# Kernel optimization log

Hardware: AMD Instinct MI355X
Metric: run time of the kernel (lower is better)

## Reference

```python
import jax, jax.numpy as jnp
import numpy as np

B, N, H = 32, 1024, 128
EPS = 1e-5


def setup_inputs() -> dict:
    key = jax.random.key(0)
    ks = jax.random.split(key, 9)
    node_embeddings = jax.random.normal(ks[0], (B, N, H), dtype=jnp.float32)
    edge_relations = jax.random.normal(ks[1], (B, N, N, 3), dtype=jnp.float32)
    adjacency = jax.random.randint(ks[2], (N, N), 0, 2, dtype=jnp.int32)
    s_msg = 1.0 / np.sqrt(H + 3)
    s_upd = 1.0 / np.sqrt(2 * H)
    W_msg = jax.random.uniform(ks[3], (H, H + 3), jnp.float32, -s_msg, s_msg)
    b_msg = jax.random.uniform(ks[4], (H,), jnp.float32, -s_msg, s_msg)
    W_upd = jax.random.uniform(ks[5], (H, 2 * H), jnp.float32, -s_upd, s_upd)
    b_upd = jax.random.uniform(ks[6], (H,), jnp.float32, -s_upd, s_upd)
    gamma = jnp.ones((H,), jnp.float32)
    beta = jnp.zeros((H,), jnp.float32)
    return {"node_embeddings": node_embeddings, "edge_relations": edge_relations,
            "adjacency": adjacency, "W_msg": W_msg, "b_msg": b_msg,
            "W_upd": W_upd, "b_upd": b_upd, "gamma": gamma, "beta": beta}


def reference(node_embeddings, edge_relations, adjacency, W_msg, b_msg, W_upd, b_upd, gamma, beta):
    # node_embeddings: [B,N,H]; edge_relations: [B,N,N,3]; adjacency: [N,N]
    b_, n_, h_ = node_embeddings.shape
    mask = (adjacency > 0).astype(node_embeddings.dtype)  # mask[j,i]=1 if i is neighbor of j
    # Split msg_nn weight: Linear(cat(h_i, e_ij)) = h_i @ W_h^T + e_ij @ W_e^T + b
    W_h = W_msg[:, :h_]   # [H,H]
    W_e = W_msg[:, h_:]   # [H,3]
    h_part = jnp.einsum('bih,oh->bio', node_embeddings, W_h)       # [B,N,H]
    msg_h = jnp.einsum('ji,bio->bjo', mask, h_part)                # aggregate sender linear part
    e_agg = jnp.einsum('bijc,ji->bjc', edge_relations, mask)       # aggregate edge feats first (memory-bound)
    msg_e = jnp.einsum('bjc,oc->bjo', e_agg, W_e)
    deg = mask.sum(axis=1)                                         # [N] in-degree of j
    messages = msg_h + msg_e + deg[None, :, None] * b_msg          # bias added once per edge
    # Dropout(0.2) is identity in inference; BatchNorm uses batch stats (training-mode math).
    upd_in = jnp.concatenate([node_embeddings, messages], axis=-1)  # [B,N,2H]
    updated = jax.nn.relu(jnp.einsum('bjk,ok->bjo', upd_in, W_upd) + b_upd)
    flat = updated.reshape(-1, h_)
    mean = flat.mean(axis=0)
    var = flat.var(axis=0)  # biased, as BatchNorm1d
    normed = (flat - mean) * jax.lax.rsqrt(var + EPS) * gamma + beta
    return normed.reshape(b_, n_, h_) + node_embeddings
```

## Files before the change

kernel.cpp:

```cpp
#include <hip/hip_runtime.h>

typedef _Float16 f16;
typedef f16 f16x4 __attribute__((ext_vector_type(4)));
typedef f16 f16x8 __attribute__((ext_vector_type(8)));
typedef float f32x4 __attribute__((ext_vector_type(4)));

#define BB 32
#define NN 1024
#define HH 128
#define ROWS (BB*NN)
#define EPS 1e-5f

__device__ __forceinline__ f16 f2h(float x) { return (f16)x; }

typedef __attribute__((address_space(1))) const void gv_t;
typedef __attribute__((address_space(3))) void lv_t;
__device__ __forceinline__ void gl_lds16(const void* g, void* l) {
  __builtin_amdgcn_global_load_lds((gv_t*)g, (lv_t*)l, 16, 0, 0);
}

__global__ __launch_bounds__(256) void prep0_k(
    const float* __restrict__ W_msg, const float* __restrict__ W_upd,
    const float* __restrict__ node, const int* __restrict__ adj,
    f16* __restrict__ Wh, f16* __restrict__ Wupd, float* __restrict__ We,
    f16* __restrict__ nodeh, f16* __restrict__ maskf, f16* __restrict__ maskT,
    float* __restrict__ e_agg, float* __restrict__ sums)
{
  const int blk = blockIdx.x, t = threadIdx.x;
  if (blk < 64) {
    const long base = (long)blk*16384 + t;
    #pragma unroll
    for (int p = 0; p < 64; p++) {
      const long idx = base + (long)p*256;
      const float4 v = ((const float4*)node)[idx];
      f16x4 hv; hv[0] = f2h(v.x); hv[1] = f2h(v.y); hv[2] = f2h(v.z); hv[3] = f2h(v.w);
      *(f16x4*)&nodeh[idx << 2] = hv;
    }
  } else if (blk < 128) {
    __shared__ f16 ldsT[128][136];
    const int tt = blk - 64, tj = tt >> 3, ti = tt & 7;
    #pragma unroll
    for (int p = 0; p < 16; p++) {
      const int q = p*256 + t;
      const int row = q >> 5, c4 = (q & 31) << 2;
      const int4 m = *(const int4*)&adj[(long)(tj*128 + row)*NN + ti*128 + c4];
      f16x4 hv;
      hv[0] = (m.x > 0) ? (f16)1.0f : (f16)0.0f;
      hv[1] = (m.y > 0) ? (f16)1.0f : (f16)0.0f;
      hv[2] = (m.z > 0) ? (f16)1.0f : (f16)0.0f;
      hv[3] = (m.w > 0) ? (f16)1.0f : (f16)0.0f;
      *(f16x4*)&maskf[(long)(tj*128 + row)*NN + ti*128 + c4] = hv;
      ldsT[c4 + 0][row] = hv[0];
      ldsT[c4 + 1][row] = hv[1];
      ldsT[c4 + 2][row] = hv[2];
      ldsT[c4 + 3][row] = hv[3];
    }
    __syncthreads();
    #pragma unroll
    for (int p = 0; p < 8; p++) {
      const int q = p*256 + t;
      const int rT = q >> 4, c8 = (q & 15) << 3;
      *(uint4*)&maskT[(long)(ti*128 + rT)*NN + tj*128 + c8] =
          *(const uint4*)&ldsT[rT][c8];
    }
  } else if (blk == 128) {
    for (int idx = t; idx < HH*HH; idx += 256) {
      const int o = idx >> 7, h = idx & 127;
      Wh[idx] = f2h(W_msg[o*131 + h]);
    }
  } else if (blk == 129) {
    for (int idx = t; idx < HH*256; idx += 256)
      Wupd[idx] = f2h(W_upd[idx]);
  } else if (blk == 130) {
    for (int idx = t; idx < HH*3; idx += 256)
      We[idx] = W_msg[(idx/3)*131 + 128 + (idx % 3)];
    if (t < 256) sums[t] = 0.f;
  } else {
    const int base = (blk - 131) * 24576 + t;
    #pragma unroll
    for (int r = 0; r < 96; r++) e_agg[base + r*256] = 0.f;
  }
}

__global__ __launch_bounds__(256) void phaseB_k(
    const f16* __restrict__ nodeh, const float* __restrict__ E,
    const f16* __restrict__ maskT, const f16* __restrict__ Wh,
    const float* __restrict__ b_msg,
    f16* __restrict__ h_part_T, float* __restrict__ e_agg)
{
  __shared__ __align__(16) char smem[16384];
  const int tid = threadIdx.x;

  if (blockIdx.x >= 256) {
    const int e   = blockIdx.x - 256;
    const int bb  = e / 96;
    const int rem = e - bb*96;
    const int seg = rem >> 5;
    const int ic  = rem & 31;
    const int i0  = ic << 5;
    const int p0  = (seg << 10) + (tid << 2);
    const int j0  = p0 / 3;
    const int r   = p0 - j0*3;
    const bool s1 = (r >= 2);
    const bool s2 = (r >= 1);
    const float* Ep = E + (long)bb*3145728 + (long)i0*3072 + p0;
    const f16*   Mp = maskT + (long)i0*NN + j0;
    float a0 = 0.f, a1 = 0.f, a2 = 0.f, a3 = 0.f;
    for (int c8 = 0; c8 < 4; c8++) {
      float4 ev[8];
      float m0v[8], m1v[8];
      #pragma unroll
      for (int v = 0; v < 8; v++)
        ev[v] = *(const float4*)(Ep + (long)(c8*8 + v)*3072);
      #pragma unroll
      for (int v = 0; v < 8; v++) {
        const long moff = (long)(c8*8 + v)*NN;
        m0v[v] = (float)Mp[moff];
        m1v[v] = (float)Mp[moff + 1];
      }
      #pragma unroll
      for (int v = 0; v < 8; v++) {
        a0 = fmaf(m0v[v],              ev[v].x, a0);
        a1 = fmaf(s1 ? m1v[v] : m0v[v], ev[v].y, a1);
        a2 = fmaf(s2 ? m1v[v] : m0v[v], ev[v].z, a2);
        a3 = fmaf(m1v[v],              ev[v].w, a3);
      }
    }
    float* ebp = e_agg + (long)bb*3072 + p0;
    atomicAdd(ebp,     a0);
    atomicAdd(ebp + 1, a1);
    atomicAdd(ebp + 2, a2);
    atomicAdd(ebp + 3, a3);
    return;
  }

  f16* As = (f16*)smem;
  f16* Bs = (f16*)(smem + 8192);
  const int g  = blockIdx.x;
  const int nt = g & 7, bb = g >> 3;
  const int nbase = nt << 7;
  const int lane = tid & 63, wave = tid >> 6;
  const int wm = (wave & 1) << 6, wn = (wave >> 1) << 6;

  f32x4 acc[2][4], acc2[2][4];
  #pragma unroll
  for (int i = 0; i < 2; i++)
    #pragma unroll
    for (int j = 0; j < 4; j++)
      #pragma unroll
      for (int r = 0; r < 4; r++) { acc[i][j][r] = 0.f; acc2[i][j][r] = 0.f; }

  for (int k0 = 0; k0 < HH; k0 += 32) {
    #pragma unroll
    for (int p = 0; p < 2; p++) {
      const int q = (p << 8) + tid;
      const int row = q >> 2, kp = (q & 3) << 3;
      gl_lds16(&Wh[(long)row*HH + k0 + kp], &As[q << 3]);
      gl_lds16(&nodeh[(long)((bb << 10) + nbase + row)*HH + k0 + kp], &Bs[q << 3]);
    }
    __syncthreads();
    f16x8 af[4], bf[4];
    #pragma unroll
    for (int i = 0; i < 4; i++) {
      af[i] = *(const f16x8*)&As[((wm + (i << 4) + (lane & 15)) << 5) + ((lane >> 4) << 3)];
      bf[i] = *(const f16x8*)&Bs[((wn + (i << 4) + (lane & 15)) << 5) + ((lane >> 4) << 3)];
    }
    #pragma unroll
    for (int i = 0; i < 2; i++)
      #pragma unroll
      for (int j = 0; j < 4; j++) {
        acc[i][j]  = __builtin_amdgcn_mfma_f32_16x16x32_f16(af[i],     bf[j], acc[i][j],  0, 0, 0);
        acc2[i][j] = __builtin_amdgcn_mfma_f32_16x16x32_f16(af[i + 2], bf[j], acc2[i][j], 0, 0, 0);
      }
    __syncthreads();
  }

  f16* out = h_part_T + (long)bb * (HH*NN);
  const int rb = (lane >> 4) << 2, cb = lane & 15;
  #pragma unroll
  for (int i = 0; i < 4; i++)
    #pragma unroll
    for (int r = 0; r < 4; r++) {
      const int gm = wm + (i << 4) + rb + r;
      const float bm = b_msg[gm];
      #pragma unroll
      for (int j = 0; j < 4; j++) {
        const int gn = nbase + wn + (j << 4) + cb;
        const float v = ((i < 2) ? acc[i][j][r] : acc2[i - 2][j][r]) + bm;
        out[(long)gm*NN + gn] = f2h(v);
      }
    }
}

__global__ __launch_bounds__(256) void gemm12_k(
    const f16* __restrict__ maskf, const f16* __restrict__ hp,
    const float* __restrict__ e_agg, const float* __restrict__ We,
    const f16* __restrict__ nodeh, const f16* __restrict__ Wupd,
    const float* __restrict__ b_upd,
    f16* __restrict__ upd, float* __restrict__ sums)
{
  const int mt = blockIdx.x, bb = blockIdx.z;
  const int jb = mt << 7;
  const long rowb = (long)bb*NN + jb;
  __shared__ f16 As[128*32];
  __shared__ f16 Bs[128*32];
  __shared__ __align__(16) char msgs_lds[128*128*2];
  __shared__ float colS[128], colQ[128];
  const int tid = threadIdx.x, lane = tid & 63, wave = tid >> 6;
  const int wm = (wave & 1) << 6, wn = (wave >> 1) << 6;
  if (tid < 128) { colS[tid] = 0.f; colQ[tid] = 0.f; }
  const int rb = (lane >> 4) << 2, cb = lane & 15;

  f32x4 acc[4][4];
  #pragma unroll
  for (int i = 0; i < 4; i++)
    #pragma unroll
    for (int j = 0; j < 4; j++)
      #pragma unroll
      for (int r = 0; r < 4; r++) acc[i][j][r] = 0.f;

  for (int k0 = 0; k0 < NN; k0 += 32) {
    #pragma unroll
    for (int p = 0; p < 2; p++) {
      const int q = (p << 8) + tid;
      const int row = q >> 2, kp = (q & 3) << 3;
      gl_lds16(&maskf[(long)(jb + row)*NN + k0 + kp], &As[q << 3]);
      gl_lds16(&hp[(long)bb*(HH*NN) + (long)row*NN + k0 + kp], &Bs[q << 3]);
    }
    __syncthreads();
    f16x8 af[4], bf[4];
    #pragma unroll
    for (int i = 0; i < 4; i++) {
      af[i] = *(const f16x8*)&As[((wm + (i << 4) + (lane & 15)) << 5) + ((lane >> 4) << 3)];
      bf[i] = *(const f16x8*)&Bs[((wn + (i << 4) + (lane & 15)) << 5) + ((lane >> 4) << 3)];
    }
    #pragma unroll
    for (int i = 0; i < 4; i++)
      #pragma unroll
      for (int j = 0; j < 4; j++)
        acc[i][j] = __builtin_amdgcn_mfma_f32_16x16x32_f16(af[i], bf[j], acc[i][j], 0, 0, 0);
    __syncthreads();
  }

  #pragma unroll
  for (int i = 0; i < 4; i++)
    #pragma unroll
    for (int r = 0; r < 4; r++) {
      const int lrow = wm + (i << 4) + rb + r;
      const long eb = (rowb + lrow)*3;
      const float e0 = e_agg[eb], e1 = e_agg[eb+1], e2 = e_agg[eb+2];
      #pragma unroll
      for (int j = 0; j < 4; j++) {
        const int col = wn + (j << 4) + cb;
        const float v = acc[i][j][r]
                      + e0*We[col*3] + e1*We[col*3+1] + e2*We[col*3+2];
        const int byte = ((lrow << 8) + (col << 1)) ^ ((lrow & 7) << 4);
        *(f16*)(msgs_lds + byte) = f2h(v);
      }
    }
  __syncthreads();

  f32x4 acc2[4][4];
  #pragma unroll
  for (int i = 0; i < 4; i++)
    #pragma unroll
    for (int j = 0; j < 4; j++)
      #pragma unroll
      for (int r = 0; r < 4; r++) acc2[i][j][r] = 0.f;

  for (int k0 = 0; k0 < 256; k0 += 32) {
    const bool fromA = (k0 < HH);
    #pragma unroll
    for (int p = 0; p < 2; p++) {
      const int q = (p << 8) + tid;
      const int row = q >> 2, kp = (q & 3) << 3;
      if (fromA)
        gl_lds16(&nodeh[(rowb + row)*HH + k0 + kp], &As[q << 3]);
      gl_lds16(&Wupd[(long)row*256 + k0 + kp], &Bs[q << 3]);
    }
    __syncthreads();
    f16x8 af[4], bf[4];
    #pragma unroll
    for (int i = 0; i < 4; i++) {
      if (fromA) {
        af[i] = *(const f16x8*)&As[((wm + (i << 4) + (lane & 15)) << 5) + ((lane >> 4) << 3)];
      } else {
        const int lrow = wm + (i << 4) + (lane & 15);
        const int byte = ((lrow << 8) + (((k0 - HH) + ((lane >> 4) << 3)) << 1))
                         ^ ((lrow & 7) << 4);
        af[i] = *(const f16x8*)(msgs_lds + byte);
      }
      bf[i] = *(const f16x8*)&Bs[((wn + (i << 4) + (lane & 15)) << 5) + ((lane >> 4) << 3)];
    }
    #pragma unroll
    for (int i = 0; i < 4; i++)
      #pragma unroll
      for (int j = 0; j < 4; j++)
        acc2[i][j] = __builtin_amdgcn_mfma_f32_16x16x32_f16(af[i], bf[j], acc2[i][j], 0, 0, 0);
    __syncthreads();
  }

  float bup[4], s[4] = {0,0,0,0}, qq[4] = {0,0,0,0};
  #pragma unroll
  for (int j = 0; j < 4; j++) bup[j] = b_upd[wn + (j << 4) + cb];
  #pragma unroll
  for (int i = 0; i < 4; i++)
    #pragma unroll
    for (int r = 0; r < 4; r++) {
      const long gm = rowb + wm + (i << 4) + rb + r;
      #pragma unroll
      for (int j = 0; j < 4; j++) {
        const int gn = wn + (j << 4) + cb;
        const float v = fmaxf(acc2[i][j][r] + bup[j], 0.f);
        upd[gm*HH + gn] = f2h(v);
        s[j] += v; qq[j] += v*v;
      }
    }
  #pragma unroll
  for (int j = 0; j < 4; j++) {
    const int gn = wn + (j << 4) + cb;
    atomicAdd(&colS[gn], s[j]);
    atomicAdd(&colQ[gn], qq[j]);
  }
  __syncthreads();
  if (tid < 128) {
    atomicAdd(&sums[tid],       colS[tid]);
    atomicAdd(&sums[128 + tid], colQ[tid]);
  }
}

__global__ __launch_bounds__(256) void final_k(const f16* __restrict__ upd,
    const float* __restrict__ node, const float* __restrict__ sums,
    const float* __restrict__ gamma, const float* __restrict__ beta,
    float* __restrict__ out)
{
  const long idx = (long)blockIdx.x*256 + threadIdx.x;
  const f16x4 u  = *(const f16x4*)&upd[idx << 2];
  const float4 nd = ((const float4*)node)[idx];
  const int ob = (idx & 31) << 2;
  const float inv = 1.0f/32768.0f;
  float4 res;
  #pragma unroll
  for (int c = 0; c < 4; c++) {
    const float m  = sums[ob + c]*inv;
    const float va = sums[128 + ob + c]*inv - m*m;
    const float sc = rsqrtf(va + EPS)*gamma[ob + c];
    ((float*)&res)[c] = ((float)u[c] - m)*sc + beta[ob + c]
                      + ((const float*)&nd)[c];
  }
  ((float4*)out)[idx] = res;
}

extern "C" void kernel_launch(void* const* d_in, const int* in_sizes, int n_in,
                              void* d_out, int out_size, void* d_ws, size_t ws_size,
                              hipStream_t stream) {
  const float* node  = (const float*)d_in[0];
  const float* E     = (const float*)d_in[1];
  const int*   adj   = (const int*)  d_in[2];
  const float* W_msg = (const float*)d_in[3];
  const float* b_msg = (const float*)d_in[4];
  const float* W_upd = (const float*)d_in[5];
  const float* b_upd = (const float*)d_in[6];
  const float* gamma = (const float*)d_in[7];
  const float* beta  = (const float*)d_in[8];
  float* out = (float*)d_out;

  char* p = (char*)d_ws;
  auto alloc = [&](size_t n) { void* r = (void*)p; p += (n + 255) & ~(size_t)255; return r; };
  f16*   h_part_T = (f16*)  alloc((size_t)BB*HH*NN*2);
  f16*   upd      = (f16*)  alloc((size_t)ROWS*HH*2);
  f16*   nodeh    = (f16*)  alloc((size_t)ROWS*HH*2);
  f16*   maskf    = (f16*)  alloc((size_t)NN*NN*2);
  f16*   maskT    = (f16*)  alloc((size_t)NN*NN*2);
  float* e_agg    = (float*)alloc((size_t)BB*NN*3*4);
  f16*   Wh       = (f16*)  alloc((size_t)HH*HH*2);
  f16*   Wupd     = (f16*)  alloc((size_t)HH*256*2);
  float* We       = (float*)alloc((size_t)HH*3*4);
  float* sums     = (float*)alloc((size_t)256*4);

  prep0_k<<<135, 256, 0, stream>>>(W_msg, W_upd, node, adj,
                                   Wh, Wupd, We, nodeh, maskf, maskT,
                                   e_agg, sums);

  phaseB_k<<<3328, 256, 0, stream>>>(nodeh, E, maskT, Wh, b_msg, h_part_T, e_agg);

  gemm12_k<<<dim3(8, 1, BB), 256, 0, stream>>>(maskf, h_part_T, e_agg, We,
                                               nodeh, Wupd, b_upd, upd, sums);

  final_k<<<4096, 256, 0, stream>>>(upd, node, sums, gamma, beta, out);
}
```

Baseline: 624.8 us.

## Double-buffer LDS tiles in gemm12 and halve edge-aggregation block count

```diff
diff --git a/kernel.cpp b/kernel.cpp
--- a/kernel.cpp
+++ b/kernel.cpp
@@ -93,11 +93,11 @@
 
   if (blockIdx.x >= 256) {
     const int e   = blockIdx.x - 256;
-    const int bb  = e / 96;
-    const int rem = e - bb*96;
-    const int seg = rem >> 5;
-    const int ic  = rem & 31;
-    const int i0  = ic << 5;
+    const int bb  = e / 48;
+    const int rem = e - bb*48;
+    const int seg = rem >> 4;
+    const int ic  = rem & 15;
+    const int i0  = ic << 6;
     const int p0  = (seg << 10) + (tid << 2);
     const int j0  = p0 / 3;
     const int r   = p0 - j0*3;
@@ -106,7 +106,7 @@
     const float* Ep = E + (long)bb*3145728 + (long)i0*3072 + p0;
     const f16*   Mp = maskT + (long)i0*NN + j0;
     float a0 = 0.f, a1 = 0.f, a2 = 0.f, a3 = 0.f;
-    for (int c8 = 0; c8 < 4; c8++) {
+    for (int c8 = 0; c8 < 8; c8++) {
       float4 ev[8];
       float m0v[8], m1v[8];
       #pragma unroll
@@ -120,10 +120,10 @@
       }
       #pragma unroll
       for (int v = 0; v < 8; v++) {
-        a0 = fmaf(m0v[v],              ev[v].x, a0);
+        a0 = fmaf(m0v[v],               ev[v].x, a0);
         a1 = fmaf(s1 ? m1v[v] : m0v[v], ev[v].y, a1);
         a2 = fmaf(s2 ? m1v[v] : m0v[v], ev[v].z, a2);
-        a3 = fmaf(m1v[v],              ev[v].w, a3);
+        a3 = fmaf(m1v[v],               ev[v].w, a3);
       }
     }
     float* ebp = e_agg + (long)bb*3072 + p0;
@@ -202,8 +202,9 @@
   const int mt = blockIdx.x, bb = blockIdx.z;
   const int jb = mt << 7;
   const long rowb = (long)bb*NN + jb;
-  __shared__ f16 As[128*32];
-  __shared__ f16 Bs[128*32];
+  const long hpbase = (long)bb*(HH*NN);
+  __shared__ f16 As[2][128*32];
+  __shared__ f16 Bs[2][128*32];
   __shared__ __align__(16) char msgs_lds[128*128*2];
   __shared__ float colS[128], colQ[128];
   const int tid = threadIdx.x, lane = tid & 63, wave = tid >> 6;
@@ -219,20 +220,26 @@
       #pragma unroll
       for (int r = 0; r < 4; r++) acc[i][j][r] = 0.f;
 
-  for (int k0 = 0; k0 < NN; k0 += 32) {
+  auto stage1 = [&](int buf, int k0) {
     #pragma unroll
     for (int p = 0; p < 2; p++) {
       const int q = (p << 8) + tid;
       const int row = q >> 2, kp = (q & 3) << 3;
-      gl_lds16(&maskf[(long)(jb + row)*NN + k0 + kp], &As[q << 3]);
-      gl_lds16(&hp[(long)bb*(HH*NN) + (long)row*NN + k0 + kp], &Bs[q << 3]);
-    }
-    __syncthreads();
+      gl_lds16(&maskf[(long)(jb + row)*NN + k0 + kp], &As[buf][q << 3]);
+      gl_lds16(&hp[hpbase + (long)row*NN + k0 + kp], &Bs[buf][q << 3]);
+    }
+  };
+
+  stage1(0, 0);
+  __syncthreads();
+  for (int t = 0; t < 32; t++) {
+    const int cur = t & 1;
+    if (t + 1 < 32) stage1(cur ^ 1, (t + 1) << 5);
     f16x8 af[4], bf[4];
     #pragma unroll
     for (int i = 0; i < 4; i++) {
-      af[i] = *(const f16x8*)&As[((wm + (i << 4) + (lane & 15)) << 5) + ((lane >> 4) << 3)];
-      bf[i] = *(const f16x8*)&Bs[((wn + (i << 4) + (lane & 15)) << 5) + ((lane >> 4) << 3)];
+      af[i] = *(const f16x8*)&As[cur][((wm + (i << 4) + (lane & 15)) << 5) + ((lane >> 4) << 3)];
+      bf[i] = *(const f16x8*)&Bs[cur][((wn + (i << 4) + (lane & 15)) << 5) + ((lane >> 4) << 3)];
     }
     #pragma unroll
     for (int i = 0; i < 4; i++)
@@ -268,29 +275,35 @@
       #pragma unroll
       for (int r = 0; r < 4; r++) acc2[i][j][r] = 0.f;
 
-  for (int k0 = 0; k0 < 256; k0 += 32) {
-    const bool fromA = (k0 < HH);
+  auto stage2 = [&](int buf, int t) {
+    const int k0 = t << 5;
     #pragma unroll
     for (int p = 0; p < 2; p++) {
       const int q = (p << 8) + tid;
       const int row = q >> 2, kp = (q & 3) << 3;
-      if (fromA)
-        gl_lds16(&nodeh[(rowb + row)*HH + k0 + kp], &As[q << 3]);
-      gl_lds16(&Wupd[(long)row*256 + k0 + kp], &Bs[q << 3]);
-    }
-    __syncthreads();
+      if (t < 4)
+        gl_lds16(&nodeh[(rowb + row)*HH + k0 + kp], &As[buf][q << 3]);
+      gl_lds16(&Wupd[(long)row*256 + k0 + kp], &Bs[buf][q << 3]);
+    }
+  };
+
+  stage2(0, 0);
+  __syncthreads();
+  for (int t = 0; t < 8; t++) {
+    const int cur = t & 1;
+    if (t + 1 < 8) stage2(cur ^ 1, t + 1);
     f16x8 af[4], bf[4];
     #pragma unroll
     for (int i = 0; i < 4; i++) {
-      if (fromA) {
-        af[i] = *(const f16x8*)&As[((wm + (i << 4) + (lane & 15)) << 5) + ((lane >> 4) << 3)];
+      if (t < 4) {
+        af[i] = *(const f16x8*)&As[cur][((wm + (i << 4) + (lane & 15)) << 5) + ((lane >> 4) << 3)];
       } else {
         const int lrow = wm + (i << 4) + (lane & 15);
-        const int byte = ((lrow << 8) + (((k0 - HH) + ((lane >> 4) << 3)) << 1))
+        const int byte = ((lrow << 8) + ((((t - 4) << 5) + ((lane >> 4) << 3)) << 1))
                          ^ ((lrow & 7) << 4);
         af[i] = *(const f16x8*)(msgs_lds + byte);
       }
-      bf[i] = *(const f16x8*)&Bs[((wn + (i << 4) + (lane & 15)) << 5) + ((lane >> 4) << 3)];
+      bf[i] = *(const f16x8*)&Bs[cur][((wn + (i << 4) + (lane & 15)) << 5) + ((lane >> 4) << 3)];
     }
     #pragma unroll
     for (int i = 0; i < 4; i++)
@@ -382,7 +395,7 @@
                                    Wh, Wupd, We, nodeh, maskf, maskT,
                                    e_agg, sums);
 
-  phaseB_k<<<3328, 256, 0, stream>>>(nodeh, E, maskT, Wh, b_msg, h_part_T, e_agg);
+  phaseB_k<<<1792, 256, 0, stream>>>(nodeh, E, maskT, Wh, b_msg, h_part_T, e_agg);
 
   gemm12_k<<<dim3(8, 1, BB), 256, 0, stream>>>(maskf, h_part_T, e_agg, We,
                                                nodeh, Wupd, b_upd, upd, sums);
```

Result: no change. 632.2 us (+1.2%).

## Fuse BatchNorm finalize into update GEMM via grid-wide atomic barrier

Applied to the files above, without the earlier changes.

```diff
diff --git a/kernel.cpp b/kernel.cpp
--- a/kernel.cpp
+++ b/kernel.cpp
@@ -24,7 +24,8 @@
     const float* __restrict__ node, const int* __restrict__ adj,
     f16* __restrict__ Wh, f16* __restrict__ Wupd, float* __restrict__ We,
     f16* __restrict__ nodeh, f16* __restrict__ maskf, f16* __restrict__ maskT,
-    float* __restrict__ e_agg, float* __restrict__ sums)
+    float* __restrict__ e_agg, float* __restrict__ sums,
+    unsigned* __restrict__ done)
 {
   const int blk = blockIdx.x, t = threadIdx.x;
   if (blk < 64) {
@@ -75,6 +76,7 @@
     for (int idx = t; idx < HH*3; idx += 256)
       We[idx] = W_msg[(idx/3)*131 + 128 + (idx % 3)];
     if (t < 256) sums[t] = 0.f;
+    if (t == 0) *done = 0u;
   } else {
     const int base = (blk - 131) * 24576 + t;
     #pragma unroll
@@ -120,10 +122,10 @@
       }
       #pragma unroll
       for (int v = 0; v < 8; v++) {
-        a0 = fmaf(m0v[v],              ev[v].x, a0);
+        a0 = fmaf(m0v[v],               ev[v].x, a0);
         a1 = fmaf(s1 ? m1v[v] : m0v[v], ev[v].y, a1);
         a2 = fmaf(s2 ? m1v[v] : m0v[v], ev[v].z, a2);
-        a3 = fmaf(m1v[v],              ev[v].w, a3);
+        a3 = fmaf(m1v[v],               ev[v].w, a3);
       }
     }
     float* ebp = e_agg + (long)bb*3072 + p0;
@@ -192,16 +194,19 @@
     }
 }
 
-__global__ __launch_bounds__(256) void gemm12_k(
+__global__ __launch_bounds__(256) void gemm12f_k(
     const f16* __restrict__ maskf, const f16* __restrict__ hp,
     const float* __restrict__ e_agg, const float* __restrict__ We,
     const f16* __restrict__ nodeh, const f16* __restrict__ Wupd,
-    const float* __restrict__ b_upd,
-    f16* __restrict__ upd, float* __restrict__ sums)
+    const float* __restrict__ b_upd, const float* __restrict__ node,
+    const float* __restrict__ gamma, const float* __restrict__ beta,
+    float* __restrict__ sums, unsigned* __restrict__ done,
+    float* __restrict__ out)
 {
   const int mt = blockIdx.x, bb = blockIdx.z;
   const int jb = mt << 7;
   const long rowb = (long)bb*NN + jb;
+  const long hpbase = (long)bb*(HH*NN);
   __shared__ f16 As[128*32];
   __shared__ f16 Bs[128*32];
   __shared__ __align__(16) char msgs_lds[128*128*2];
@@ -225,7 +230,7 @@
       const int q = (p << 8) + tid;
       const int row = q >> 2, kp = (q & 3) << 3;
       gl_lds16(&maskf[(long)(jb + row)*NN + k0 + kp], &As[q << 3]);
-      gl_lds16(&hp[(long)bb*(HH*NN) + (long)row*NN + k0 + kp], &Bs[q << 3]);
+      gl_lds16(&hp[hpbase + (long)row*NN + k0 + kp], &Bs[q << 3]);
     }
     __syncthreads();
     f16x8 af[4], bf[4];
@@ -306,16 +311,13 @@
   #pragma unroll
   for (int i = 0; i < 4; i++)
     #pragma unroll
-    for (int r = 0; r < 4; r++) {
-      const long gm = rowb + wm + (i << 4) + rb + r;
+    for (int r = 0; r < 4; r++)
       #pragma unroll
       for (int j = 0; j < 4; j++) {
-        const int gn = wn + (j << 4) + cb;
         const float v = fmaxf(acc2[i][j][r] + bup[j], 0.f);
-        upd[gm*HH + gn] = f2h(v);
+        acc2[i][j][r] = v;
         s[j] += v; qq[j] += v*v;
       }
-    }
   #pragma unroll
   for (int j = 0; j < 4; j++) {
     const int gn = wn + (j << 4) + cb;
@@ -327,28 +329,37 @@
     atomicAdd(&sums[tid],       colS[tid]);
     atomicAdd(&sums[128 + tid], colQ[tid]);
   }
-}
-
-__global__ __launch_bounds__(256) void final_k(const f16* __restrict__ upd,
-    const float* __restrict__ node, const float* __restrict__ sums,
-    const float* __restrict__ gamma, const float* __restrict__ beta,
-    float* __restrict__ out)
-{
-  const long idx = (long)blockIdx.x*256 + threadIdx.x;
-  const f16x4 u  = *(const f16x4*)&upd[idx << 2];
-  const float4 nd = ((const float4*)node)[idx];
-  const int ob = (idx & 31) << 2;
+
+  __threadfence();
+  __syncthreads();
+  if (tid == 0) {
+    __hip_atomic_fetch_add(done, 1u, __ATOMIC_ACQ_REL, __HIP_MEMORY_SCOPE_AGENT);
+    while (__hip_atomic_load(done, __ATOMIC_ACQUIRE, __HIP_MEMORY_SCOPE_AGENT) < 256u)
+      __builtin_amdgcn_s_sleep(1);
+  }
+  __syncthreads();
+  if (tid < 128) {
+    colS[tid] = __hip_atomic_load(&sums[tid], __ATOMIC_RELAXED, __HIP_MEMORY_SCOPE_AGENT);
+    colQ[tid] = __hip_atomic_load(&sums[128 + tid], __ATOMIC_RELAXED, __HIP_MEMORY_SCOPE_AGENT);
+  }
+  __syncthreads();
+
   const float inv = 1.0f/32768.0f;
-  float4 res;
-  #pragma unroll
-  for (int c = 0; c < 4; c++) {
-    const float m  = sums[ob + c]*inv;
-    const float va = sums[128 + ob + c]*inv - m*m;
-    const float sc = rsqrtf(va + EPS)*gamma[ob + c];
-    ((float*)&res)[c] = ((float)u[c] - m)*sc + beta[ob + c]
-                      + ((const float*)&nd)[c];
-  }
-  ((float4*)out)[idx] = res;
+  #pragma unroll
+  for (int j = 0; j < 4; j++) {
+    const int gn = wn + (j << 4) + cb;
+    const float m  = colS[gn]*inv;
+    const float va = colQ[gn]*inv - m*m;
+    const float sc = rsqrtf(va + EPS)*gamma[gn];
+    const float bt = beta[gn];
+    #pragma unroll
+    for (int i = 0; i < 4; i++)
+      #pragma unroll
+      for (int r = 0; r < 4; r++) {
+        const long gm = rowb + wm + (i << 4) + rb + r;
+        out[gm*HH + gn] = (acc2[i][j][r] - m)*sc + bt + node[gm*HH + gn];
+      }
+  }
 }
 
 extern "C" void kernel_launch(void* const* d_in, const int* in_sizes, int n_in,
@@ -368,7 +379,6 @@
   char* p = (char*)d_ws;
   auto alloc = [&](size_t n) { void* r = (void*)p; p += (n + 255) & ~(size_t)255; return r; };
   f16*   h_part_T = (f16*)  alloc((size_t)BB*HH*NN*2);
-  f16*   upd      = (f16*)  alloc((size_t)ROWS*HH*2);
   f16*   nodeh    = (f16*)  alloc((size_t)ROWS*HH*2);
   f16*   maskf    = (f16*)  alloc((size_t)NN*NN*2);
   f16*   maskT    = (f16*)  alloc((size_t)NN*NN*2);
@@ -377,15 +387,15 @@
   f16*   Wupd     = (f16*)  alloc((size_t)HH*256*2);
   float* We       = (float*)alloc((size_t)HH*3*4);
   float* sums     = (float*)alloc((size_t)256*4);
+  unsigned* done  = (unsigned*)alloc(256);
 
   prep0_k<<<135, 256, 0, stream>>>(W_msg, W_upd, node, adj,
                                    Wh, Wupd, We, nodeh, maskf, maskT,
-                                   e_agg, sums);
+                                   e_agg, sums, done);
 
   phaseB_k<<<3328, 256, 0, stream>>>(nodeh, E, maskT, Wh, b_msg, h_part_T, e_agg);
 
-  gemm12_k<<<dim3(8, 1, BB), 256, 0, stream>>>(maskf, h_part_T, e_agg, We,
-                                               nodeh, Wupd, b_upd, upd, sums);
-
-  final_k<<<4096, 256, 0, stream>>>(upd, node, sums, gamma, beta, out);
+  gemm12f_k<<<dim3(8, 1, BB), 256, 0, stream>>>(maskf, h_part_T, e_agg, We,
+                                                nodeh, Wupd, b_upd, node,
+                                                gamma, beta, sums, done, out);
 }
```

New measurement: 649.4 us. 1.04x slower.
